# Kernel tuning notes

Measured on AMD Instinct MI355X. Metric: run time of the kernel, lower is better.

Reference implementation:

```python
import jax, jax.numpy as jnp
import numpy as np

B, T, N, C = 1, 2, 10000, 64
H, Co = 4, 64
E = 160000
NEG_SLOPE = 0.2
LN_EPS = 1e-5


def setup_inputs() -> dict:
    key = jax.random.key(0)
    ks = jax.random.split(key, 8)
    s_in = 1.0 / np.sqrt(C)
    s_att = 1.0 / np.sqrt(Co)
    s_proj = 1.0 / np.sqrt(H * Co)
    return {
        "x": jax.random.normal(ks[0], (B, T, N, C), jnp.float32),
        "edge_index": jax.random.randint(ks[1], (2, E), 0, N, dtype=jnp.int32),
        "W_l": jax.random.normal(ks[2], (C, H * Co), jnp.float32) * s_in,
        "b_l": jnp.zeros((H * Co,), jnp.float32),
        "W_r": jax.random.normal(ks[3], (C, H * Co), jnp.float32) * s_in,
        "b_r": jnp.zeros((H * Co,), jnp.float32),
        "att": jax.random.normal(ks[4], (H, Co), jnp.float32) * s_att,
        "bias": jnp.zeros((H * Co,), jnp.float32),
        "W_proj": jax.random.normal(ks[5], (H * Co, Co), jnp.float32) * s_proj,
        "b_proj": jnp.zeros((Co,), jnp.float32),
        "ln_gamma": jnp.ones((Co,), jnp.float32),
        "ln_beta": jnp.zeros((Co,), jnp.float32),
    }


def reference(x, edge_index, W_l, b_l, W_r, b_r, att, bias, W_proj, b_proj, ln_gamma, ln_beta):
    src, dst = edge_index[0], edge_index[1]
    # node transforms: [B,T,N,H,Co]
    x_l = (x @ W_l + b_l).reshape(B, T, N, H, Co)
    x_r = (x @ W_r + b_r).reshape(B, T, N, H, Co)
    # per-edge gathers: [B,T,E,H,Co]
    x_j = x_l[:, :, src]  # source-side features (messages)
    x_i = x_r[:, :, dst]  # target-side features
    m = jax.nn.leaky_relu(x_i + x_j, NEG_SLOPE)
    alpha = jnp.einsum('bteho,ho->bteh', m, att)  # [B,T,E,H]
    # segment softmax over edges grouped by target node (edge axis leading)
    a = jnp.moveaxis(alpha, 2, 0)  # [E,B,T,H]
    amax = jax.lax.stop_gradient(jax.ops.segment_max(a, dst, num_segments=N))
    a = jnp.exp(a - amax[dst])
    denom = jax.ops.segment_sum(a, dst, num_segments=N)
    attn = a / denom[dst]  # [E,B,T,H]
    # weighted messages scattered to target nodes
    msg = jnp.moveaxis(x_j, 2, 0) * attn[..., None]  # [E,B,T,H,Co]
    agg = jax.ops.segment_sum(msg, dst, num_segments=N)  # [N,B,T,H,Co]
    out = jnp.moveaxis(agg, 0, 2).reshape(B, T, N, H * Co) + bias
    x_mha = jax.nn.relu(out)
    # projection + identity residual (in_channels == out_channels)
    x_sam = x_mha @ W_proj + b_proj + x
    mu = jnp.mean(x_sam, axis=-1, keepdims=True)
    var = jnp.var(x_sam, axis=-1, keepdims=True)
    y = (x_sam - mu) * jax.lax.rsqrt(var + LN_EPS) * ln_gamma + ln_beta
    return jax.nn.relu(y)
```

## Files before the change

### kernel.cpp

```cpp
#include <hip/hip_runtime.h>

#define T_  2
#define N_  10000
#define C_  64
#define H_  4
#define Co_ 64
#define E_  160000
#define HC_ 256
#define PAD_ 48
#define NEG_SLOPE 0.2f
#define LN_EPS 1e-5f
#define SCAT_BLOCKS (E_ / 256)
#define GEMM_BLOCKS (T_ * N_ / 32)

typedef float v2f __attribute__((ext_vector_type(2)));

#if __has_builtin(__builtin_elementwise_fma)
#define PKFMA(a, b, c) __builtin_elementwise_fma((a), (b), (c))
#else
#define PKFMA(a, b, c) ((a) * (b) + (c))
#endif

__device__ __forceinline__ v2f v2(float x, float y) { v2f r; r.x = x; r.y = y; return r; }
__device__ __forceinline__ v2f sp(float x) { v2f r; r.x = x; r.y = x; return r; }

__device__ __forceinline__ float bf2f(unsigned short u) {
    return __uint_as_float((unsigned)u << 16);
}
__device__ __forceinline__ unsigned short f2bf(float f) {
    const unsigned u = __float_as_uint(f);
    return (unsigned short)((u + 0x7FFFu + ((u >> 16) & 1u)) >> 16);
}
__device__ __forceinline__ float4 u2f4(ushort4 u) {
    return make_float4(bf2f(u.x), bf2f(u.y), bf2f(u.z), bf2f(u.w));
}

__device__ __forceinline__ void red16x4(float& p0, float& p1, float& p2, float& p3) {
    asm("s_nop 1\n\t"
        "v_add_f32_dpp %0, %0, %0 quad_perm:[1,0,3,2] row_mask:0xf bank_mask:0xf\n\t"
        "v_add_f32_dpp %1, %1, %1 quad_perm:[1,0,3,2] row_mask:0xf bank_mask:0xf\n\t"
        "v_add_f32_dpp %2, %2, %2 quad_perm:[1,0,3,2] row_mask:0xf bank_mask:0xf\n\t"
        "v_add_f32_dpp %3, %3, %3 quad_perm:[1,0,3,2] row_mask:0xf bank_mask:0xf\n\t"
        "v_add_f32_dpp %0, %0, %0 quad_perm:[2,3,0,1] row_mask:0xf bank_mask:0xf\n\t"
        "v_add_f32_dpp %1, %1, %1 quad_perm:[2,3,0,1] row_mask:0xf bank_mask:0xf\n\t"
        "v_add_f32_dpp %2, %2, %2 quad_perm:[2,3,0,1] row_mask:0xf bank_mask:0xf\n\t"
        "v_add_f32_dpp %3, %3, %3 quad_perm:[2,3,0,1] row_mask:0xf bank_mask:0xf\n\t"
        "v_add_f32_dpp %0, %0, %0 row_half_mirror row_mask:0xf bank_mask:0xf\n\t"
        "v_add_f32_dpp %1, %1, %1 row_half_mirror row_mask:0xf bank_mask:0xf\n\t"
        "v_add_f32_dpp %2, %2, %2 row_half_mirror row_mask:0xf bank_mask:0xf\n\t"
        "v_add_f32_dpp %3, %3, %3 row_half_mirror row_mask:0xf bank_mask:0xf\n\t"
        "v_add_f32_dpp %0, %0, %0 row_mirror row_mask:0xf bank_mask:0xf\n\t"
        "v_add_f32_dpp %1, %1, %1 row_mirror row_mask:0xf bank_mask:0xf\n\t"
        "v_add_f32_dpp %2, %2, %2 row_mirror row_mask:0xf bank_mask:0xf\n\t"
        "v_add_f32_dpp %3, %3, %3 row_mirror row_mask:0xf bank_mask:0xf"
        : "+v"(p0), "+v"(p1), "+v"(p2), "+v"(p3));
}

__device__ __forceinline__ float edot2(const v2f xa, const v2f xb,
                                       const v2f aa, const v2f ab, const float4 c) {
    v2f u = v2(c.x, c.y) + xa;
    v2f v = v2(c.z, c.w) + xb;
    v2f lu = __builtin_elementwise_max(u, u * 0.2f);
    v2f lv = __builtin_elementwise_max(v, v * 0.2f);
    v2f p = PKFMA(lv, ab, lu * aa);
    return p.x + p.y;
}

__device__ __forceinline__ void group_update(
        const v2f xa, const v2f xb, const v2f aa, const v2f ab,
        const float4 c0, const float4 c1, const float4 c2, const float4 c3,
        int k, int cnt, float& m, float& s, float4& acc) {
    float p0 = edot2(xa, xb, aa, ab, c0);
    float p1 = edot2(xa, xb, aa, ab, c1);
    float p2 = edot2(xa, xb, aa, ab, c2);
    float p3 = edot2(xa, xb, aa, ab, c3);
    red16x4(p0, p1, p2, p3);
    if (k + 1 >= cnt) p1 = -INFINITY;
    if (k + 2 >= cnt) p2 = -INFINITY;
    if (k + 3 >= cnt) p3 = -INFINITY;
    const float gm = fmaxf(fmaxf(p0, p1), fmaxf(p2, p3));
    const float mn = fmaxf(m, gm);
    const float sc = __expf(m - mn);
    const float w0 = __expf(p0 - mn);
    const float w1 = __expf(p1 - mn);
    const float w2 = __expf(p2 - mn);
    const float w3 = __expf(p3 - mn);
    s = fmaf(s, sc, w0 + w1 + w2 + w3);
    v2f q01 = v2(c3.x, c3.y) * w3;
    q01 = PKFMA(v2(c2.x, c2.y), sp(w2), q01);
    q01 = PKFMA(v2(c1.x, c1.y), sp(w1), q01);
    q01 = PKFMA(v2(c0.x, c0.y), sp(w0), q01);
    v2f r01 = PKFMA(v2(acc.x, acc.y), sp(sc), q01);
    v2f q23 = v2(c3.z, c3.w) * w3;
    q23 = PKFMA(v2(c2.z, c2.w), sp(w2), q23);
    q23 = PKFMA(v2(c1.z, c1.w), sp(w1), q23);
    q23 = PKFMA(v2(c0.z, c0.w), sp(w0), q23);
    v2f r23 = PKFMA(v2(acc.z, acc.w), sp(sc), q23);
    acc.x = r01.x; acc.y = r01.y; acc.z = r23.x; acc.w = r23.y;
    m = mn;
}

__global__ __launch_bounds__(256) void scat_gemm(
        const int* __restrict__ src, const int* __restrict__ dst,
        int* __restrict__ cursor, unsigned short* __restrict__ perm,
        const float* __restrict__ x, const float* __restrict__ Wl,
        const float* __restrict__ bl, const float* __restrict__ Wr,
        const float* __restrict__ br, unsigned short* __restrict__ xlb,
        float* __restrict__ xr) {
    __shared__ float4 xs[32 * 16];
    const int tid = threadIdx.x;
    if (blockIdx.x < SCAT_BLOCKS) {
        const int e = blockIdx.x * 256 + tid;
        const int d = dst[e];
        const int pos = atomicAdd(&cursor[d], 1);
        if (pos < PAD_) perm[d * PAD_ + pos] = (unsigned short)src[e];
        return;
    }
    const int r0 = (blockIdx.x - SCAT_BLOCKS) * 32;
    xs[tid]       = ((const float4*)(x + (size_t)r0 * C_))[tid];
    xs[256 + tid] = ((const float4*)(x + (size_t)r0 * C_))[256 + tid];
    __syncthreads();

    const int wv    = tid >> 6;
    const int mat   = wv >> 1;
    const int rbase = (wv & 1) << 4;
    const int col4  = tid & 63;
    const float* W  = mat ? Wr : Wl;
    const float4 b4 = ((const float4*)(mat ? br : bl))[col4];

    float4 acc[16];
    #pragma unroll
    for (int r = 0; r < 16; ++r) acc[r] = b4;

    #pragma unroll 2
    for (int c4 = 0; c4 < 16; ++c4) {
        const float4 w0 = ((const float4*)(W + (size_t)(c4 * 4 + 0) * HC_))[col4];
        const float4 w1 = ((const float4*)(W + (size_t)(c4 * 4 + 1) * HC_))[col4];
        const float4 w2 = ((const float4*)(W + (size_t)(c4 * 4 + 2) * HC_))[col4];
        const float4 w3 = ((const float4*)(W + (size_t)(c4 * 4 + 3) * HC_))[col4];
        #pragma unroll
        for (int r = 0; r < 16; ++r) {
            const float4 xv = xs[(rbase + r) * 16 + c4];
            acc[r].x = fmaf(xv.x, w0.x, acc[r].x);
            acc[r].y = fmaf(xv.x, w0.y, acc[r].y);
            acc[r].z = fmaf(xv.x, w0.z, acc[r].z);
            acc[r].w = fmaf(xv.x, w0.w, acc[r].w);
            acc[r].x = fmaf(xv.y, w1.x, acc[r].x);
            acc[r].y = fmaf(xv.y, w1.y, acc[r].y);
            acc[r].z = fmaf(xv.y, w1.z, acc[r].z);
            acc[r].w = fmaf(xv.y, w1.w, acc[r].w);
            acc[r].x = fmaf(xv.z, w2.x, acc[r].x);
            acc[r].y = fmaf(xv.z, w2.y, acc[r].y);
            acc[r].z = fmaf(xv.z, w2.z, acc[r].z);
            acc[r].w = fmaf(xv.z, w2.w, acc[r].w);
            acc[r].x = fmaf(xv.w, w3.x, acc[r].x);
            acc[r].y = fmaf(xv.w, w3.y, acc[r].y);
            acc[r].z = fmaf(xv.w, w3.z, acc[r].z);
            acc[r].w = fmaf(xv.w, w3.w, acc[r].w);
        }
    }
    if (mat) {
        #pragma unroll
        for (int r = 0; r < 16; ++r)
            ((float4*)(xr + (size_t)(r0 + rbase + r) * HC_))[col4] = acc[r];
    } else {
        #pragma unroll
        for (int r = 0; r < 16; ++r) {
            ushort4 u;
            u.x = f2bf(acc[r].x); u.y = f2bf(acc[r].y);
            u.z = f2bf(acc[r].z); u.w = f2bf(acc[r].w);
            ((ushort4*)(xlb + (size_t)(r0 + rbase + r) * HC_))[col4] = u;
        }
    }
}

__global__ __launch_bounds__(256, 4) void node_proj(
        const unsigned short* __restrict__ xlb, const float* __restrict__ xr,
        const float* __restrict__ att, const unsigned short* __restrict__ perm,
        const int* __restrict__ cursor, const float* __restrict__ bias,
        const float* __restrict__ Wp, const float* __restrict__ bp,
        const float* __restrict__ x, const float* __restrict__ gamma,
        const float* __restrict__ beta, float* __restrict__ out) {
    __shared__ float sh[4][2][HC_];
    const int wv   = threadIdx.x >> 6;
    const int lane = threadIdx.x & 63;
    const int n    = blockIdx.x * 4 + wv;
    const int deg  = min(cursor[n], PAD_);
    const float4 av  = ((const float4*)att)[lane];
    const float4 xi0 = ((const float4*)&xr[(size_t)n * HC_])[lane];
    const float4 xi1 = ((const float4*)&xr[((size_t)N_ + n) * HC_])[lane];
    const int myidx  = (lane < deg) ? (int)perm[n * PAD_ + lane] : 0;
    const unsigned short* xl1 = xlb + (size_t)N_ * HC_;

    const v2f xa = v2(xi0.x, xi0.y), xb = v2(xi0.z, xi0.w);
    const v2f ya = v2(xi1.x, xi1.y), yb = v2(xi1.z, xi1.w);
    const v2f aa = v2(av.x, av.y),   ab = v2(av.z, av.w);

    float m0 = -INFINITY, s0 = 0.f, m1 = -INFINITY, s1 = 0.f;
    float4 a0 = make_float4(0.f, 0.f, 0.f, 0.f), a1 = a0;

    ushort4 b0, b1, b2, b3, b4, b5, b6, b7;
    auto fetch = [&](int kk) {
        const int i0 = __builtin_amdgcn_readlane(myidx, kk + 0);
        const int i1 = __builtin_amdgcn_readlane(myidx, kk + 1);
        const int i2 = __builtin_amdgcn_readlane(myidx, kk + 2);
        const int i3 = __builtin_amdgcn_readlane(myidx, kk + 3);
        b0 = ((const ushort4*)&xlb[(size_t)i0 * HC_])[lane];
        b1 = ((const ushort4*)&xlb[(size_t)i1 * HC_])[lane];
        b2 = ((const ushort4*)&xlb[(size_t)i2 * HC_])[lane];
        b3 = ((const ushort4*)&xlb[(size_t)i3 * HC_])[lane];
        b4 = ((const ushort4*)&xl1[(size_t)i0 * HC_])[lane];
        b5 = ((const ushort4*)&xl1[(size_t)i1 * HC_])[lane];
        b6 = ((const ushort4*)&xl1[(size_t)i2 * HC_])[lane];
        b7 = ((const ushort4*)&xl1[(size_t)i3 * HC_])[lane];
    };
    if (deg > 0) fetch(0);
    for (int k = 0; k < deg; k += 4) {
        const float4 c0 = u2f4(b0), c1 = u2f4(b1), c2 = u2f4(b2), c3 = u2f4(b3);
        const float4 d0 = u2f4(b4), d1 = u2f4(b5), d2 = u2f4(b6), d3 = u2f4(b7);
        if (k + 4 < deg) fetch(k + 4);
        group_update(xa, xb, aa, ab, c0, c1, c2, c3, k, deg, m0, s0, a0);
        group_update(ya, yb, aa, ab, d0, d1, d2, d3, k, deg, m1, s1, a1);
    }

    const float4 bias4 = ((const float4*)bias)[lane];
    {
        const float i0v = (deg > 0) ? 1.f / s0 : 0.f;
        const float i1v = (deg > 0) ? 1.f / s1 : 0.f;
        float4 v;
        v.x = fmaxf(fmaf(a0.x, i0v, bias4.x), 0.f);
        v.y = fmaxf(fmaf(a0.y, i0v, bias4.y), 0.f);
        v.z = fmaxf(fmaf(a0.z, i0v, bias4.z), 0.f);
        v.w = fmaxf(fmaf(a0.w, i0v, bias4.w), 0.f);
        ((float4*)&sh[wv][0][0])[lane] = v;
        v.x = fmaxf(fmaf(a1.x, i1v, bias4.x), 0.f);
        v.y = fmaxf(fmaf(a1.y, i1v, bias4.y), 0.f);
        v.z = fmaxf(fmaf(a1.z, i1v, bias4.z), 0.f);
        v.w = fmaxf(fmaf(a1.w, i1v, bias4.w), 0.f);
        ((float4*)&sh[wv][1][0])[lane] = v;
    }
    asm volatile("s_waitcnt lgkmcnt(0)" ::: "memory");

    const int o = lane;
    const float* sh0 = &sh[wv][0][0];
    const float* sh1 = &sh[wv][1][0];
    v2f P0 = v2(0.f, 0.f), P1 = v2(0.f, 0.f);
    #pragma unroll 4
    for (int k = 0; k < HC_; k += 4) {
        const float w0 = Wp[(k + 0) * Co_ + o];
        const float w1 = Wp[(k + 1) * Co_ + o];
        const float w2 = Wp[(k + 2) * Co_ + o];
        const float w3 = Wp[(k + 3) * Co_ + o];
        const float4 s0v = ((const float4*)sh0)[k >> 2];
        const float4 s1v = ((const float4*)sh1)[k >> 2];
        P0 = PKFMA(v2(s0v.x, s0v.y), v2(w0, w1), P0);
        P0 = PKFMA(v2(s0v.z, s0v.w), v2(w2, w3), P0);
        P1 = PKFMA(v2(s1v.x, s1v.y), v2(w0, w1), P1);
        P1 = PKFMA(v2(s1v.z, s1v.w), v2(w2, w3), P1);
    }
    const float bpo = bp[o];
    float p0 = P0.x + P0.y + bpo + x[(size_t)n * C_ + o];
    float p1 = P1.x + P1.y + bpo + x[((size_t)N_ + n) * C_ + o];

    const float go = gamma[o], bo = beta[o];
    {
        float s1r = p0;
        #pragma unroll
        for (int off = 1; off < 64; off <<= 1) s1r += __shfl_xor(s1r, off, 64);
        const float mu0 = s1r * (1.f / 64.f);
        const float dv0 = p0 - mu0;
        float s2r = dv0 * dv0;
        #pragma unroll
        for (int off = 1; off < 64; off <<= 1) s2r += __shfl_xor(s2r, off, 64);
        out[(size_t)n * C_ + o] =
            fmaxf(dv0 * rsqrtf(s2r * (1.f / 64.f) + LN_EPS) * go + bo, 0.f);

        float t1r = p1;
        #pragma unroll
        for (int off = 1; off < 64; off <<= 1) t1r += __shfl_xor(t1r, off, 64);
        const float mu1 = t1r * (1.f / 64.f);
        const float dv1 = p1 - mu1;
        float t2r = dv1 * dv1;
        #pragma unroll
        for (int off = 1; off < 64; off <<= 1) t2r += __shfl_xor(t2r, off, 64);
        out[((size_t)N_ + n) * C_ + o] =
            fmaxf(dv1 * rsqrtf(t2r * (1.f / 64.f) + LN_EPS) * go + bo, 0.f);
    }
}

extern "C" void kernel_launch(void* const* d_in, const int* in_sizes, int n_in,
                              void* d_out, int out_size, void* d_ws, size_t ws_size,
                              hipStream_t stream) {
    const float* x    = (const float*)d_in[0];
    const int*   ei   = (const int*)  d_in[1];
    const float* Wl   = (const float*)d_in[2];
    const float* bl   = (const float*)d_in[3];
    const float* Wr   = (const float*)d_in[4];
    const float* br   = (const float*)d_in[5];
    const float* att  = (const float*)d_in[6];
    const float* bias = (const float*)d_in[7];
    const float* Wp   = (const float*)d_in[8];
    const float* bp   = (const float*)d_in[9];
    const float* gam  = (const float*)d_in[10];
    const float* bet  = (const float*)d_in[11];
    const int* src = ei;
    const int* dst = ei + E_;

    char* ws = (char*)d_ws;
    unsigned short* xlb  = (unsigned short*)ws;
    float*          xr   = (float*)(xlb + (size_t)T_ * N_ * HC_);
    int*            cursor = (int*)(xr + (size_t)T_ * N_ * HC_);
    unsigned short* perm   = (unsigned short*)(cursor + N_);

    hipMemsetAsync(cursor, 0, N_ * sizeof(int), stream);
    scat_gemm<<<SCAT_BLOCKS + GEMM_BLOCKS, 256, 0, stream>>>(
        src, dst, cursor, perm, x, Wl, bl, Wr, br, xlb, xr);
    node_proj<<<N_ / 4, 256, 0, stream>>>(xlb, xr, att, perm, cursor, bias,
                                          Wp, bp, x, gam, bet, (float*)d_out);
}
```

Baseline: 162.4 us.

## Split projection GEMM across waves by K and pack FMAs in node GEMM

The node-transform GEMM now accumulates with packed two-wide FMAs instead of scalar FMAs, halving the FMA instruction count. In the aggregation kernel the output projection is restructured: each wave computes partial products over a quarter of K for all 8 rows in the block, then partials are reduced through shared memory. This cuts per-wave W_proj reads by four and reuses each weight across 8 rows, at the cost of two block barriers and extra LDS traffic.

```diff
diff --git a/kernel.cpp b/kernel.cpp
--- a/kernel.cpp
+++ b/kernel.cpp
@@ -128,9 +128,9 @@
     const float* W  = mat ? Wr : Wl;
     const float4 b4 = ((const float4*)(mat ? br : bl))[col4];
 
-    float4 acc[16];
+    v2f accA[16], accB[16];
     #pragma unroll
-    for (int r = 0; r < 16; ++r) acc[r] = b4;
+    for (int r = 0; r < 16; ++r) { accA[r] = v2(b4.x, b4.y); accB[r] = v2(b4.z, b4.w); }
 
     #pragma unroll 2
     for (int c4 = 0; c4 < 16; ++c4) {
@@ -138,37 +138,36 @@
         const float4 w1 = ((const float4*)(W + (size_t)(c4 * 4 + 1) * HC_))[col4];
         const float4 w2 = ((const float4*)(W + (size_t)(c4 * 4 + 2) * HC_))[col4];
         const float4 w3 = ((const float4*)(W + (size_t)(c4 * 4 + 3) * HC_))[col4];
+        const v2f w0A = v2(w0.x, w0.y), w0B = v2(w0.z, w0.w);
+        const v2f w1A = v2(w1.x, w1.y), w1B = v2(w1.z, w1.w);
+        const v2f w2A = v2(w2.x, w2.y), w2B = v2(w2.z, w2.w);
+        const v2f w3A = v2(w3.x, w3.y), w3B = v2(w3.z, w3.w);
         #pragma unroll
         for (int r = 0; r < 16; ++r) {
             const float4 xv = xs[(rbase + r) * 16 + c4];
-            acc[r].x = fmaf(xv.x, w0.x, acc[r].x);
-            acc[r].y = fmaf(xv.x, w0.y, acc[r].y);
-            acc[r].z = fmaf(xv.x, w0.z, acc[r].z);
-            acc[r].w = fmaf(xv.x, w0.w, acc[r].w);
-            acc[r].x = fmaf(xv.y, w1.x, acc[r].x);
-            acc[r].y = fmaf(xv.y, w1.y, acc[r].y);
-            acc[r].z = fmaf(xv.y, w1.z, acc[r].z);
-            acc[r].w = fmaf(xv.y, w1.w, acc[r].w);
-            acc[r].x = fmaf(xv.z, w2.x, acc[r].x);
-            acc[r].y = fmaf(xv.z, w2.y, acc[r].y);
-            acc[r].z = fmaf(xv.z, w2.z, acc[r].z);
-            acc[r].w = fmaf(xv.z, w2.w, acc[r].w);
-            acc[r].x = fmaf(xv.w, w3.x, acc[r].x);
-            acc[r].y = fmaf(xv.w, w3.y, acc[r].y);
-            acc[r].z = fmaf(xv.w, w3.z, acc[r].z);
-            acc[r].w = fmaf(xv.w, w3.w, acc[r].w);
+            accA[r] = PKFMA(sp(xv.x), w0A, accA[r]);
+            accB[r] = PKFMA(sp(xv.x), w0B, accB[r]);
+            accA[r] = PKFMA(sp(xv.y), w1A, accA[r]);
+            accB[r] = PKFMA(sp(xv.y), w1B, accB[r]);
+            accA[r] = PKFMA(sp(xv.z), w2A, accA[r]);
+            accB[r] = PKFMA(sp(xv.z), w2B, accB[r]);
+            accA[r] = PKFMA(sp(xv.w), w3A, accA[r]);
+            accB[r] = PKFMA(sp(xv.w), w3B, accB[r]);
         }
     }
     if (mat) {
         #pragma unroll
-        for (int r = 0; r < 16; ++r)
-            ((float4*)(xr + (size_t)(r0 + rbase + r) * HC_))[col4] = acc[r];
+        for (int r = 0; r < 16; ++r) {
+            float4 o4;
+            o4.x = accA[r].x; o4.y = accA[r].y; o4.z = accB[r].x; o4.w = accB[r].y;
+            ((float4*)(xr + (size_t)(r0 + rbase + r) * HC_))[col4] = o4;
+        }
     } else {
         #pragma unroll
         for (int r = 0; r < 16; ++r) {
             ushort4 u;
-            u.x = f2bf(acc[r].x); u.y = f2bf(acc[r].y);
-            u.z = f2bf(acc[r].z); u.w = f2bf(acc[r].w);
+            u.x = f2bf(accA[r].x); u.y = f2bf(accA[r].y);
+            u.z = f2bf(accB[r].x); u.w = f2bf(accB[r].y);
             ((ushort4*)(xlb + (size_t)(r0 + rbase + r) * HC_))[col4] = u;
         }
     }
@@ -181,7 +180,8 @@
         const float* __restrict__ Wp, const float* __restrict__ bp,
         const float* __restrict__ x, const float* __restrict__ gamma,
         const float* __restrict__ beta, float* __restrict__ out) {
-    __shared__ float sh[4][2][HC_];
+    __shared__ float sh_act[8][HC_];
+    __shared__ float sh_part[4][8][Co_];
     const int wv   = threadIdx.x >> 6;
     const int lane = threadIdx.x & 63;
     const int n    = blockIdx.x * 4 + wv;
@@ -232,35 +232,48 @@
         v.y = fmaxf(fmaf(a0.y, i0v, bias4.y), 0.f);
         v.z = fmaxf(fmaf(a0.z, i0v, bias4.z), 0.f);
         v.w = fmaxf(fmaf(a0.w, i0v, bias4.w), 0.f);
-        ((float4*)&sh[wv][0][0])[lane] = v;
+        ((float4*)&sh_act[2 * wv + 0][0])[lane] = v;
         v.x = fmaxf(fmaf(a1.x, i1v, bias4.x), 0.f);
         v.y = fmaxf(fmaf(a1.y, i1v, bias4.y), 0.f);
         v.z = fmaxf(fmaf(a1.z, i1v, bias4.z), 0.f);
         v.w = fmaxf(fmaf(a1.w, i1v, bias4.w), 0.f);
-        ((float4*)&sh[wv][1][0])[lane] = v;
-    }
-    asm volatile("s_waitcnt lgkmcnt(0)" ::: "memory");
+        ((float4*)&sh_act[2 * wv + 1][0])[lane] = v;
+    }
+    __syncthreads();
+
+    v2f part[8];
+    #pragma unroll
+    for (int r = 0; r < 8; ++r) part[r] = v2(0.f, 0.f);
+    {
+        const int kq = wv * 16;
+        #pragma unroll 4
+        for (int k4 = 0; k4 < 16; ++k4) {
+            const int k = (kq + k4) * 4;
+            const float w0 = Wp[(size_t)(k + 0) * Co_ + lane];
+            const float w1 = Wp[(size_t)(k + 1) * Co_ + lane];
+            const float w2 = Wp[(size_t)(k + 2) * Co_ + lane];
+            const float w3 = Wp[(size_t)(k + 3) * Co_ + lane];
+            const v2f w01 = v2(w0, w1), w23 = v2(w2, w3);
+            #pragma unroll
+            for (int r = 0; r < 8; ++r) {
+                const float4 a = ((const float4*)&sh_act[r][0])[kq + k4];
+                part[r] = PKFMA(v2(a.x, a.y), w01, part[r]);
+                part[r] = PKFMA(v2(a.z, a.w), w23, part[r]);
+            }
+        }
+    }
+    #pragma unroll
+    for (int r = 0; r < 8; ++r) sh_part[wv][r][lane] = part[r].x + part[r].y;
+    __syncthreads();
 
     const int o = lane;
-    const float* sh0 = &sh[wv][0][0];
-    const float* sh1 = &sh[wv][1][0];
-    v2f P0 = v2(0.f, 0.f), P1 = v2(0.f, 0.f);
-    #pragma unroll 4
-    for (int k = 0; k < HC_; k += 4) {
-        const float w0 = Wp[(k + 0) * Co_ + o];
-        const float w1 = Wp[(k + 1) * Co_ + o];
-        const float w2 = Wp[(k + 2) * Co_ + o];
-        const float w3 = Wp[(k + 3) * Co_ + o];
-        const float4 s0v = ((const float4*)sh0)[k >> 2];
-        const float4 s1v = ((const float4*)sh1)[k >> 2];
-        P0 = PKFMA(v2(s0v.x, s0v.y), v2(w0, w1), P0);
-        P0 = PKFMA(v2(s0v.z, s0v.w), v2(w2, w3), P0);
-        P1 = PKFMA(v2(s1v.x, s1v.y), v2(w0, w1), P1);
-        P1 = PKFMA(v2(s1v.z, s1v.w), v2(w2, w3), P1);
-    }
     const float bpo = bp[o];
-    float p0 = P0.x + P0.y + bpo + x[(size_t)n * C_ + o];
-    float p1 = P1.x + P1.y + bpo + x[((size_t)N_ + n) * C_ + o];
+    float p0 = sh_part[0][2 * wv + 0][o] + sh_part[1][2 * wv + 0][o]
+             + sh_part[2][2 * wv + 0][o] + sh_part[3][2 * wv + 0][o]
+             + bpo + x[(size_t)n * C_ + o];
+    float p1 = sh_part[0][2 * wv + 1][o] + sh_part[1][2 * wv + 1][o]
+             + sh_part[2][2 * wv + 1][o] + sh_part[3][2 * wv + 1][o]
+             + bpo + x[((size_t)N_ + n) * C_ + o];
 
     const float go = gamma[o], bo = beta[o];
     {
```

After: 164.4 us. Within noise of the previous version (+1.2%).
